# Kernel optimization log

Hardware: AMD Instinct MI355X
Metric: run time of the kernel (lower is better)

Reference implementation:

```python
import jax, jax.numpy as jnp
import numpy as np

B, T, V, D = 128, 512, 8000, 256
H = D // 2   # per-direction LSTM hidden
L = 4        # label_dim


def setup_inputs() -> dict:
    key = jax.random.key(0)
    ks = jax.random.split(key, 16)
    s = 0.1
    pad_seq = jax.random.randint(ks[0], (B, T), 0, V)
    lens = jax.random.randint(ks[1], (B,), 1, T + 1)
    lens = lens.at[0].set(T)  # padded length == max(lens), as pad_packed_sequence would give
    emb = (jax.random.normal(ks[2], (V, D)) * s).at[0].set(0.0)  # padding_idx=0
    return {
        "pad_seq": pad_seq, "lens": lens, "emb": emb,
        "W_ih_f": jax.random.normal(ks[3], (4 * H, D)) * s,
        "W_hh_f": jax.random.normal(ks[4], (4 * H, H)) * s,
        "b_ih_f": jax.random.normal(ks[5], (4 * H,)) * s,
        "b_hh_f": jax.random.normal(ks[6], (4 * H,)) * s,
        "W_ih_b": jax.random.normal(ks[7], (4 * H, D)) * s,
        "W_hh_b": jax.random.normal(ks[8], (4 * H, H)) * s,
        "b_ih_b": jax.random.normal(ks[9], (4 * H,)) * s,
        "b_hh_b": jax.random.normal(ks[10], (4 * H,)) * s,
        "W_lab": jax.random.normal(ks[11], (L, D)) * s,
        "b_lab": jax.random.normal(ks[12], (L,)) * s,
        "transitions": jax.random.normal(ks[13], (L, L)),
        "from_BOS": jax.random.normal(ks[14], (L,)),
        "to_EOS": jax.random.normal(ks[15], (L,)),
    }


def _lstm(xs_t, mask_t, Wih, Whh, bih, bhh, reverse):
    """Masked unidirectional LSTM over time-major xs_t [T,B,D]; emulates
    pack_padded_sequence semantics (state frozen and output zeroed at pads)."""
    nb, nh = xs_t.shape[1], Whh.shape[1]

    def step(carry, inp):
        h, c = carry
        x_t, m_t = inp  # [B,D], [B,1] bool
        g = x_t @ Wih.T + bih + h @ Whh.T + bhh
        i, f, gg, o = jnp.split(g, 4, axis=-1)
        c2 = jax.nn.sigmoid(f) * c + jax.nn.sigmoid(i) * jnp.tanh(gg)
        h2 = jax.nn.sigmoid(o) * jnp.tanh(c2)
        h = jnp.where(m_t, h2, h)
        c = jnp.where(m_t, c2, c)
        return (h, c), jnp.where(m_t, h2, 0.0)

    init = (jnp.zeros((nb, nh), xs_t.dtype), jnp.zeros((nb, nh), xs_t.dtype))
    _, ys = jax.lax.scan(step, init, (xs_t, mask_t), reverse=reverse)
    return ys  # [T,B,H]


def reference(pad_seq, lens, emb, W_ih_f, W_hh_f, b_ih_f, b_hh_f,
              W_ih_b, W_hh_b, b_ih_b, b_hh_b, W_lab, b_lab,
              transitions, from_BOS, to_EOS):
    b, t = pad_seq.shape
    x = emb[pad_seq]                       # [B,T,D]
    xs_t = jnp.transpose(x, (1, 0, 2))     # [T,B,D]
    mask_t = (jnp.arange(t)[:, None] < lens[None, :])[:, :, None]  # [T,B,1]

    hf = _lstm(xs_t, mask_t, W_ih_f, W_hh_f, b_ih_f, b_hh_f, reverse=False)
    hb = _lstm(xs_t, mask_t, W_ih_b, W_hh_b, b_ih_b, b_hh_b, reverse=True)
    h = jnp.concatenate([hf, hb], axis=-1)           # [T,B,D]
    scores = h @ W_lab.T + b_lab                     # [T,B,L] emissions

    # --- Viterbi forward pass ---
    best0 = from_BOS[None, :] + scores[0]            # [B,L]

    def vstep(best, inp):
        ti, e = inp                                  # step index, emissions [B,L]
        smat = best[:, :, None] + e[:, None, :] + transitions[None]  # [B,prev,cur]
        valid = (lens > ti)[:, None]
        nb = jnp.where(valid, smat.max(axis=1), best)
        return nb, jnp.argmax(smat, axis=1)          # backtrace [B,L]

    bestT, bt = jax.lax.scan(vstep, best0, (jnp.arange(1, t), scores[1:]))
    final_vec = bestT + to_EOS[None, :]              # [B,L]
    last_lab = jnp.argmax(final_vec, axis=1)         # [B]

    # --- backtrace: label[t] = bt[t][label[t+1]] for t < len-1 ---
    bt_pad = jnp.concatenate([bt, jnp.zeros((1,) + bt.shape[1:], bt.dtype)], axis=0)  # [T,B,L]

    def bstep(cur, inp):
        ti, bt_t = inp
        cand = jnp.take_along_axis(bt_t, cur[:, None], axis=1)[:, 0]
        cur = jnp.where(ti == lens - 1, last_lab,
                        jnp.where(ti < lens - 1, cand, cur))
        return cur, cur

    _, labs = jax.lax.scan(bstep, jnp.zeros((b,), last_lab.dtype),
                           (jnp.arange(t), bt_pad), reverse=True)
    labels = labs.T  # [B,T]
    len_bool = jnp.arange(t)[None, :] < lens[:, None]
    return labels * len_bool
```

## Files before the change

### kernel.cpp

```cpp
#include <hip/hip_runtime.h>
#include <math.h>

#define VOCAB 8000
#define BATCH 128
#define TMAX  512
#define DIM   256
#define HID   128
#define G4    512
#define NCOL  1024

__global__ __launch_bounds__(256) void embw_gemm(
    const float* __restrict__ emb,
    const float* __restrict__ Wf, const float* __restrict__ Wb,
    const float* __restrict__ bihf, const float* __restrict__ bhhf,
    const float* __restrict__ bihb, const float* __restrict__ bhhb,
    float* __restrict__ embW) {
  __shared__ float As[32][132];
  __shared__ float Bs[32][132];
  const int tid = threadIdx.x;
  const int m0 = blockIdx.x * 128;
  const int n0 = blockIdx.y * 128;
  const int tx = tid & 15, ty = tid >> 4;
  const int lrow = tid >> 1;
  const int lseg = (tid & 1) * 16;
  const float* Wsrc = (n0 < 512) ? Wf : Wb;
  const int nbase = (n0 < 512) ? n0 : (n0 - 512);

  float acc[8][8];
  #pragma unroll
  for (int i = 0; i < 8; ++i)
    #pragma unroll
    for (int jj = 0; jj < 8; ++jj) acc[i][jj] = 0.f;

  for (int k0 = 0; k0 < 256; k0 += 32) {
    const int gm = m0 + lrow;
    #pragma unroll
    for (int q = 0; q < 4; ++q) {
      float4 v = make_float4(0.f, 0.f, 0.f, 0.f);
      if (gm < VOCAB) v = *(const float4*)(emb + (size_t)gm * 256 + k0 + lseg + 4 * q);
      As[lseg + 4*q + 0][lrow] = v.x;
      As[lseg + 4*q + 1][lrow] = v.y;
      As[lseg + 4*q + 2][lrow] = v.z;
      As[lseg + 4*q + 3][lrow] = v.w;
    }
    #pragma unroll
    for (int q = 0; q < 4; ++q) {
      float4 v = *(const float4*)(Wsrc + (size_t)(nbase + lrow) * 256 + k0 + lseg + 4 * q);
      Bs[lseg + 4*q + 0][lrow] = v.x;
      Bs[lseg + 4*q + 1][lrow] = v.y;
      Bs[lseg + 4*q + 2][lrow] = v.z;
      Bs[lseg + 4*q + 3][lrow] = v.w;
    }
    __syncthreads();
    #pragma unroll
    for (int k = 0; k < 32; ++k) {
      float4 av0 = *(const float4*)&As[k][ty * 8];
      float4 av1 = *(const float4*)&As[k][ty * 8 + 4];
      float4 bv0 = *(const float4*)&Bs[k][tx * 4];
      float4 bv1 = *(const float4*)&Bs[k][64 + tx * 4];
      float a[8]  = {av0.x, av0.y, av0.z, av0.w, av1.x, av1.y, av1.z, av1.w};
      float bb[8] = {bv0.x, bv0.y, bv0.z, bv0.w, bv1.x, bv1.y, bv1.z, bv1.w};
      #pragma unroll
      for (int i = 0; i < 8; ++i)
        #pragma unroll
        for (int jj = 0; jj < 8; ++jj)
          acc[i][jj] += a[i] * bb[jj];
    }
    __syncthreads();
  }

  float bias[8];
  #pragma unroll
  for (int jj = 0; jj < 8; ++jj) {
    int n = n0 + ((jj < 4) ? (tx * 4 + jj) : (64 + tx * 4 + (jj - 4)));
    bias[jj] = (n < 512) ? (bihf[n] + bhhf[n]) : (bihb[n - 512] + bhhb[n - 512]);
  }
  #pragma unroll
  for (int i = 0; i < 8; ++i) {
    int gm = m0 + ty * 8 + i;
    if (gm >= VOCAB) continue;
    float4 v0 = make_float4(acc[i][0] + bias[0], acc[i][1] + bias[1],
                            acc[i][2] + bias[2], acc[i][3] + bias[3]);
    float4 v1 = make_float4(acc[i][4] + bias[4], acc[i][5] + bias[5],
                            acc[i][6] + bias[6], acc[i][7] + bias[7]);
    *(float4*)(embW + (size_t)gm * NCOL + n0 + tx * 4) = v0;
    *(float4*)(embW + (size_t)gm * NCOL + n0 + 64 + tx * 4) = v1;
  }
}

#define REP8(M) M(0) M(1) M(2) M(3) M(4) M(5) M(6) M(7)
#define REP8G(M,G) M(G,0) M(G,1) M(G,2) M(G,3) M(G,4) M(G,5) M(G,6) M(G,7)

__global__ __launch_bounds__(512)
__attribute__((amdgpu_waves_per_eu(2, 2)))
void lstm_rec(
    const int* __restrict__ pad_seq, const int* __restrict__ lens,
    const float* __restrict__ Whh_f, const float* __restrict__ Whh_b,
    const float* __restrict__ embW, const float* __restrict__ W_lab,
    float* __restrict__ e_part) {
  const int dir = blockIdx.x & 1;
  const int b   = blockIdx.x >> 1;
  const int tid = threadIdx.x;
  const int j   = tid >> 2;
  const int q   = tid & 3;
  const int parity = q & 1;
  const int half   = (q >> 1) & 1;

  __shared__ float ring[8][4][36];
  __shared__ float wls[4][132];
  __shared__ int   tok[TMAX];

  tok[tid] = pad_seq[b * TMAX + tid];
  wls[tid >> 7][tid & 127] = W_lab[(tid >> 7) * DIM + dir * HID + (tid & 127)];
  if (tid < 144) ((float*)ring)[tid] = 0.f;

  const int len = lens[b];
  const float* __restrict__ Whh = dir ? Whh_b : Whh_f;

  const float4* wr0 = (const float4*)(Whh + (size_t)(0 * HID + j) * HID + 32 * q);
  const float4* wr1 = (const float4*)(Whh + (size_t)(1 * HID + j) * HID + 32 * q);
  const float4* wr2 = (const float4*)(Whh + (size_t)(2 * HID + j) * HID + 32 * q);
  const float4* wr3 = (const float4*)(Whh + (size_t)(3 * HID + j) * HID + 32 * q);
#define DECLW(G,I)                                                      \
  float w##G##_##I##_0, w##G##_##I##_1, w##G##_##I##_2, w##G##_##I##_3; \
  { float4 t = wr##G[I];                                                \
    w##G##_##I##_0 = t.x; w##G##_##I##_1 = t.y;                         \
    w##G##_##I##_2 = t.z; w##G##_##I##_3 = t.w; }                       \
  asm volatile("" : "+v"(w##G##_##I##_0));                              \
  asm volatile("" : "+v"(w##G##_##I##_1));                              \
  asm volatile("" : "+v"(w##G##_##I##_2));                              \
  asm volatile("" : "+v"(w##G##_##I##_3));
  REP8G(DECLW,0) REP8G(DECLW,1) REP8G(DECLW,2) REP8G(DECLW,3)
#undef DECLW

  float c = 0.f;
  const float ascale = (q == 2) ? 2.f : 1.f;
  const float* __restrict__ ecol = embW + dir * G4 + (q * HID + j);
  float* __restrict__ ep = e_part + (size_t)(dir * BATCH + b) * TMAX * 4;

  __syncthreads();

  float xb0, xb1, xb2, xb3, xb4, xb5, xb6, xb7;
#define PRE(r) { const int ss = nbase + r; xb##r = 0.f;                 \
    if (ss < len) {                                                     \
      const int tt = dir ? (len - 1 - ss) : ss;                         \
      xb##r = ecol[(size_t)tok[tt] * NCOL]; } }
  { const int nbase = 0; REP8(PRE) }

#define MACC(G,I)                                         \
    a##G##0 = fmaf(hv##I.x, w##G##_##I##_0, a##G##0);     \
    a##G##1 = fmaf(hv##I.y, w##G##_##I##_1, a##G##1);     \
    a##G##2 = fmaf(hv##I.z, w##G##_##I##_2, a##G##2);     \
    a##G##3 = fmaf(hv##I.w, w##G##_##I##_3, a##G##3);

#define STEP(r, XW)                                                     \
  {                                                                     \
    const float4* h4 = (const float4*)&ring[r][q][0];                   \
    float4 hv0 = h4[0], hv1 = h4[1], hv2 = h4[2], hv3 = h4[3];          \
    float4 hv4 = h4[4], hv5 = h4[5], hv6 = h4[6], hv7 = h4[7];          \
    float a00=0.f,a01=0.f,a02=0.f,a03=0.f;                              \
    float a10=0.f,a11=0.f,a12=0.f,a13=0.f;                              \
    float a20=0.f,a21=0.f,a22=0.f,a23=0.f;                              \
    float a30=0.f,a31=0.f,a32=0.f,a33=0.f;                              \
    REP8G(MACC,0) REP8G(MACC,1) REP8G(MACC,2) REP8G(MACC,3)             \
    const float p0 = (a00+a01)+(a02+a03);                               \
    const float p1 = (a10+a11)+(a12+a13);                               \
    const float p2 = (a20+a21)+(a22+a23);                               \
    const float p3 = (a30+a31)+(a32+a33);                               \
          \
    const float klo = parity ? p1 : p0, slo = parity ? p0 : p1;         \
    const float khi = parity ? p3 : p2, shi = parity ? p2 : p3;         \
    const float alo = klo + __shfl_xor(slo, 1);                         \
    const float ahi = khi + __shfl_xor(shi, 1);                         \
    const float kb = half ? ahi : alo, sb = half ? alo : ahi;           \
    const float tot = kb + __shfl_xor(sb, 2);                           \
    const float aa = tot + (XW);                                        \
    const float sg = 1.f / (1.f + __expf(-ascale * aa));                \
    const float act = (q == 2) ? (2.f * sg - 1.f) : sg;                 \
    const float e1 = __shfl_xor(act, 1);                                \
    const float e2 = __shfl_xor(act, 2);                                \
    const float e3 = __shfl_xor(e1, 2);                                 \
    const float ev  = parity ? e1 : act, od  = parity ? act : e1;       \
    const float ev2 = parity ? e3 : e2,  od2 = parity ? e2 : e3;        \
    const float ig = half ? ev2 : ev, fg = half ? od2 : od;             \
    const float gt = half ? ev : ev2, og = half ? od : od2;             \
    c = fg * c + ig * gt;                                               \
    const float s2 = 1.f / (1.f + __expf(-2.f * c));                    \
    const float hh = og * (2.f * s2 - 1.f);                             \
    if (q == 0) ring[(r + 1) & 7][j >> 5][j & 31] = hh;                 \
    __syncthreads();                                                    \
  }

  for (int s0 = 0; s0 < len; s0 += 8) {
    const int cnt = (len - s0 < 8) ? (len - s0) : 8;
    STEP(0, xb0)
    if (cnt > 1) STEP(1, xb1)
    if (cnt > 2) STEP(2, xb2)
    if (cnt > 3) STEP(3, xb3)
    if (cnt > 4) STEP(4, xb4)
    if (cnt > 5) STEP(5, xb5)
    if (cnt > 6) STEP(6, xb6)
    if (cnt > 7) STEP(7, xb7)
    { const int nbase = s0 + 8; REP8(PRE) }
    {
      const int r = tid >> 6, l = (tid >> 4) & 3, sub = tid & 15;
      if (r < cnt) {
        const float4* hp = (const float4*)&ring[(r + 1) & 7][sub >> 2][8 * (sub & 3)];
        const float4 h0 = hp[0], h1 = hp[1];
        const float4* wp = (const float4*)&wls[l][8 * sub];
        const float4 u0 = wp[0], u1 = wp[1];
        float d = h0.x*u0.x + h0.y*u0.y + h0.z*u0.z + h0.w*u0.w
                + h1.x*u1.x + h1.y*u1.y + h1.z*u1.z + h1.w*u1.w;
        d += __shfl_xor(d, 1); d += __shfl_xor(d, 2);
        d += __shfl_xor(d, 4); d += __shfl_xor(d, 8);
        if (sub == 0) {
          const int ss = s0 + r;
          const int tt = dir ? (len - 1 - ss) : ss;
          ep[tt * 4 + l] = d;
        }
      }
    }
    asm volatile("" : "+v"(xb0), "+v"(xb1), "+v"(xb2), "+v"(xb3),
                      "+v"(xb4), "+v"(xb5), "+v"(xb6), "+v"(xb7));
    __syncthreads();
  }
#undef STEP
#undef MACC
#undef PRE
}

__global__ __launch_bounds__(512) void viterbi_k(
    const int* __restrict__ lens, const float* __restrict__ e_part,
    const float* __restrict__ b_lab, const float* __restrict__ trans,
    const float* __restrict__ from_BOS, const float* __restrict__ to_EOS,
    int* __restrict__ out) {
  const int b = blockIdx.x;
  const int tid = threadIdx.x;
  __shared__ float sc[TMAX][4];
  __shared__ unsigned btm[TMAX];
  __shared__ int labs[TMAX];
  const int len = lens[b];

  if (tid < len) {
    const float4 f  = *(const float4*)(e_part + ((size_t)b * TMAX + tid) * 4);
    const float4 g2 = *(const float4*)(e_part + ((size_t)(BATCH + b) * TMAX + tid) * 4);
    const float4 bl = *(const float4*)b_lab;
    sc[tid][0] = f.x + g2.x + bl.x;
    sc[tid][1] = f.y + g2.y + bl.y;
    sc[tid][2] = f.z + g2.z + bl.z;
    sc[tid][3] = f.w + g2.w + bl.w;
  }
  __syncthreads();

  if (tid < 4) {
    const int l = tid;
    float trc0 = trans[0 * 4 + l], trc1 = trans[1 * 4 + l];
    float trc2 = trans[2 * 4 + l], trc3 = trans[3 * 4 + l];
    float best = from_BOS[l] + sc[0][l];
    float e_next = sc[1][l];
    for (int ti = 1; ti < len; ++ti) {
      const float e = e_next;
      e_next = sc[(ti + 1 < TMAX) ? ti + 1 : ti][l];
      const float b0 = __shfl(best, 0);
      const float b1 = __shfl(best, 1);
      const float b2 = __shfl(best, 2);
      const float b3 = __shfl(best, 3);
      float m = (b0 + e) + trc0; int arg = 0;
      float v;
      v = (b1 + e) + trc1; if (v > m) { m = v; arg = 1; }
      v = (b2 + e) + trc2; if (v > m) { m = v; arg = 2; }
      v = (b3 + e) + trc3; if (v > m) { m = v; arg = 3; }
      best = m;
      unsigned av = ((unsigned)arg) << (8 * l);
      av |= __shfl_xor(av, 1);
      av |= __shfl_xor(av, 2);
      if (l == 0) btm[ti] = av;
    }
    const float f0 = __shfl(best, 0) + to_EOS[0];
    const float f1 = __shfl(best, 1) + to_EOS[1];
    const float f2 = __shfl(best, 2) + to_EOS[2];
    const float f3 = __shfl(best, 3) + to_EOS[3];
    if (l == 0) {
      float m = f0; int last = 0;
      if (f1 > m) { m = f1; last = 1; }
      if (f2 > m) { m = f2; last = 2; }
      if (f3 > m) { m = f3; last = 3; }
      labs[len - 1] = last;
      int cur = last;
      #pragma unroll 4
      for (int ti = len - 2; ti >= 0; --ti) {
        cur = (int)((btm[ti + 1] >> (8 * cur)) & 255u);
        labs[ti] = cur;
      }
    }
  }
  __syncthreads();
  out[b * TMAX + tid] = (tid < len) ? labs[tid] : 0;
}

extern "C" void kernel_launch(void* const* d_in, const int* in_sizes, int n_in,
                              void* d_out, int out_size, void* d_ws, size_t ws_size,
                              hipStream_t stream) {
  const int*   pad_seq  = (const int*)d_in[0];
  const int*   lens     = (const int*)d_in[1];
  const float* emb      = (const float*)d_in[2];
  const float* W_ih_f   = (const float*)d_in[3];
  const float* W_hh_f   = (const float*)d_in[4];
  const float* b_ih_f   = (const float*)d_in[5];
  const float* b_hh_f   = (const float*)d_in[6];
  const float* W_ih_b   = (const float*)d_in[7];
  const float* W_hh_b   = (const float*)d_in[8];
  const float* b_ih_b   = (const float*)d_in[9];
  const float* b_hh_b   = (const float*)d_in[10];
  const float* W_lab    = (const float*)d_in[11];
  const float* b_lab    = (const float*)d_in[12];
  const float* trans    = (const float*)d_in[13];
  const float* from_BOS = (const float*)d_in[14];
  const float* to_EOS   = (const float*)d_in[15];
  int* out = (int*)d_out;

  float* embW   = (float*)d_ws;
  float* e_part = embW + (size_t)VOCAB * NCOL;

  embw_gemm<<<dim3(63, 8), 256, 0, stream>>>(emb, W_ih_f, W_ih_b,
                                             b_ih_f, b_hh_f, b_ih_b, b_hh_b, embW);
  lstm_rec<<<dim3(2 * BATCH), 512, 0, stream>>>(pad_seq, lens, W_hh_f, W_hh_b,
                                                embW, W_lab, e_part);
  viterbi_k<<<dim3(BATCH), 512, 0, stream>>>(lens, e_part, b_lab, trans,
                                             from_BOS, to_EOS, out);
}
```

Baseline: 628.9 us.

## Use packed FP32 FMA in the GEMM and LSTM recurrence, simplify gate reduction

Switches the embedding-weight GEMM inner product and the LSTM hidden-state matvec to two-wide float vectors so the compiler can emit packed FP32 FMAs (v_pk_fma_f32), halving the FMA instruction count. The recurrent weights are pinned in register pairs through double bitcasts. The gate reduction no longer uses parity/half select shuffles. Every lane now butterfly-reduces all four gate sums with 8 shuffles and computes all four activations redundantly, instead of one activation followed by a redistribution. This trades more shuffles and transcendentals per lane for fewer selects and a shorter dependency chain on the serial recurrence path.

```diff
diff --git a/kernel.cpp b/kernel.cpp
--- a/kernel.cpp
+++ b/kernel.cpp
@@ -8,6 +8,16 @@
 #define HID   128
 #define G4    512
 #define NCOL  1024
+
+typedef float v2f __attribute__((ext_vector_type(2)));
+
+__device__ __forceinline__ v2f fma2(v2f a, v2f b, v2f c) {
+#if __has_builtin(__builtin_elementwise_fma)
+  return __builtin_elementwise_fma(a, b, c);
+#else
+  v2f r; r.x = fmaf(a.x, b.x, c.x); r.y = fmaf(a.y, b.y, c.y); return r;
+#endif
+}
 
 __global__ __launch_bounds__(256) void embw_gemm(
     const float* __restrict__ emb,
@@ -26,11 +36,11 @@
   const float* Wsrc = (n0 < 512) ? Wf : Wb;
   const int nbase = (n0 < 512) ? n0 : (n0 - 512);
 
-  float acc[8][8];
+  v2f acc2[8][4];
   #pragma unroll
   for (int i = 0; i < 8; ++i)
     #pragma unroll
-    for (int jj = 0; jj < 8; ++jj) acc[i][jj] = 0.f;
+    for (int jj = 0; jj < 4; ++jj) { acc2[i][jj].x = 0.f; acc2[i][jj].y = 0.f; }
 
   for (int k0 = 0; k0 < 256; k0 += 32) {
     const int gm = m0 + lrow;
@@ -58,13 +68,18 @@
       float4 av1 = *(const float4*)&As[k][ty * 8 + 4];
       float4 bv0 = *(const float4*)&Bs[k][tx * 4];
       float4 bv1 = *(const float4*)&Bs[k][64 + tx * 4];
-      float a[8]  = {av0.x, av0.y, av0.z, av0.w, av1.x, av1.y, av1.z, av1.w};
-      float bb[8] = {bv0.x, bv0.y, bv0.z, bv0.w, bv1.x, bv1.y, bv1.z, bv1.w};
+      float a8[8] = {av0.x, av0.y, av0.z, av0.w, av1.x, av1.y, av1.z, av1.w};
+      v2f b20, b21, b22, b23;
+      b20.x = bv0.x; b20.y = bv0.y;  b21.x = bv0.z; b21.y = bv0.w;
+      b22.x = bv1.x; b22.y = bv1.y;  b23.x = bv1.z; b23.y = bv1.w;
       #pragma unroll
-      for (int i = 0; i < 8; ++i)
-        #pragma unroll
-        for (int jj = 0; jj < 8; ++jj)
-          acc[i][jj] += a[i] * bb[jj];
+      for (int i = 0; i < 8; ++i) {
+        v2f ai; ai.x = a8[i]; ai.y = a8[i];
+        acc2[i][0] = fma2(ai, b20, acc2[i][0]);
+        acc2[i][1] = fma2(ai, b21, acc2[i][1]);
+        acc2[i][2] = fma2(ai, b22, acc2[i][2]);
+        acc2[i][3] = fma2(ai, b23, acc2[i][3]);
+      }
     }
     __syncthreads();
   }
@@ -79,17 +94,21 @@
   for (int i = 0; i < 8; ++i) {
     int gm = m0 + ty * 8 + i;
     if (gm >= VOCAB) continue;
-    float4 v0 = make_float4(acc[i][0] + bias[0], acc[i][1] + bias[1],
-                            acc[i][2] + bias[2], acc[i][3] + bias[3]);
-    float4 v1 = make_float4(acc[i][4] + bias[4], acc[i][5] + bias[5],
-                            acc[i][6] + bias[6], acc[i][7] + bias[7]);
+    float4 v0 = make_float4(acc2[i][0].x + bias[0], acc2[i][0].y + bias[1],
+                            acc2[i][1].x + bias[2], acc2[i][1].y + bias[3]);
+    float4 v1 = make_float4(acc2[i][2].x + bias[4], acc2[i][2].y + bias[5],
+                            acc2[i][3].x + bias[6], acc2[i][3].y + bias[7]);
     *(float4*)(embW + (size_t)gm * NCOL + n0 + tx * 4) = v0;
     *(float4*)(embW + (size_t)gm * NCOL + n0 + 64 + tx * 4) = v1;
   }
 }
 
 #define REP8(M) M(0) M(1) M(2) M(3) M(4) M(5) M(6) M(7)
-#define REP8G(M,G) M(G,0) M(G,1) M(G,2) M(G,3) M(G,4) M(G,5) M(G,6) M(G,7)
+#define REPD(M,G) M(G,0,0,1) M(G,1,2,3) M(G,2,4,5) M(G,3,6,7) \
+                  M(G,4,8,9) M(G,5,10,11) M(G,6,12,13) M(G,7,14,15)
+#define REPM(M,G) M(G,0,A) M(G,1,B) M(G,2,A) M(G,3,B) M(G,4,A) M(G,5,B) \
+  M(G,6,A) M(G,7,B) M(G,8,A) M(G,9,B) M(G,10,A) M(G,11,B) M(G,12,A) \
+  M(G,13,B) M(G,14,A) M(G,15,B)
 
 __global__ __launch_bounds__(512)
 __attribute__((amdgpu_waves_per_eu(2, 2)))
@@ -103,8 +122,6 @@
   const int tid = threadIdx.x;
   const int j   = tid >> 2;
   const int q   = tid & 3;
-  const int parity = q & 1;
-  const int half   = (q >> 1) & 1;
 
   __shared__ float ring[8][4][36];
   __shared__ float wls[4][132];
@@ -121,20 +138,21 @@
   const float4* wr1 = (const float4*)(Whh + (size_t)(1 * HID + j) * HID + 32 * q);
   const float4* wr2 = (const float4*)(Whh + (size_t)(2 * HID + j) * HID + 32 * q);
   const float4* wr3 = (const float4*)(Whh + (size_t)(3 * HID + j) * HID + 32 * q);
-#define DECLW(G,I)                                                      \
-  float w##G##_##I##_0, w##G##_##I##_1, w##G##_##I##_2, w##G##_##I##_3; \
+#define DECLW(G,I,PA,PB)                                                \
+  v2f wp##G##_##PA, wp##G##_##PB;                                       \
   { float4 t = wr##G[I];                                                \
-    w##G##_##I##_0 = t.x; w##G##_##I##_1 = t.y;                         \
-    w##G##_##I##_2 = t.z; w##G##_##I##_3 = t.w; }                       \
-  asm volatile("" : "+v"(w##G##_##I##_0));                              \
-  asm volatile("" : "+v"(w##G##_##I##_1));                              \
-  asm volatile("" : "+v"(w##G##_##I##_2));                              \
-  asm volatile("" : "+v"(w##G##_##I##_3));
-  REP8G(DECLW,0) REP8G(DECLW,1) REP8G(DECLW,2) REP8G(DECLW,3)
+    v2f vA; vA.x = t.x; vA.y = t.y;                                     \
+    v2f vB; vB.x = t.z; vB.y = t.w;                                     \
+    double dA = __builtin_bit_cast(double, vA);                         \
+    double dB = __builtin_bit_cast(double, vB);                         \
+    asm volatile("" : "+v"(dA));                                        \
+    asm volatile("" : "+v"(dB));                                        \
+    wp##G##_##PA = __builtin_bit_cast(v2f, dA);                         \
+    wp##G##_##PB = __builtin_bit_cast(v2f, dB); }
+  REPD(DECLW,0) REPD(DECLW,1) REPD(DECLW,2) REPD(DECLW,3)
 #undef DECLW
 
   float c = 0.f;
-  const float ascale = (q == 2) ? 2.f : 1.f;
   const float* __restrict__ ecol = embW + dir * G4 + (q * HID + j);
   float* __restrict__ ep = e_part + (size_t)(dir * BATCH + b) * TMAX * 4;
 
@@ -147,43 +165,42 @@
       xb##r = ecol[(size_t)tok[tt] * NCOL]; } }
   { const int nbase = 0; REP8(PRE) }
 
-#define MACC(G,I)                                         \
-    a##G##0 = fmaf(hv##I.x, w##G##_##I##_0, a##G##0);     \
-    a##G##1 = fmaf(hv##I.y, w##G##_##I##_1, a##G##1);     \
-    a##G##2 = fmaf(hv##I.z, w##G##_##I##_2, a##G##2);     \
-    a##G##3 = fmaf(hv##I.w, w##G##_##I##_3, a##G##3);
+#define MACC(G,K,AB) ac##G##AB = fma2(hp##K, wp##G##_##K, ac##G##AB);
+#define HPAIR(K,F,S0,S1) v2f hp##K; hp##K.x = F.S0; hp##K.y = F.S1;
 
 #define STEP(r, XW)                                                     \
   {                                                                     \
     const float4* h4 = (const float4*)&ring[r][q][0];                   \
-    float4 hv0 = h4[0], hv1 = h4[1], hv2 = h4[2], hv3 = h4[3];          \
-    float4 hv4 = h4[4], hv5 = h4[5], hv6 = h4[6], hv7 = h4[7];          \
-    float a00=0.f,a01=0.f,a02=0.f,a03=0.f;                              \
-    float a10=0.f,a11=0.f,a12=0.f,a13=0.f;                              \
-    float a20=0.f,a21=0.f,a22=0.f,a23=0.f;                              \
-    float a30=0.f,a31=0.f,a32=0.f,a33=0.f;                              \
-    REP8G(MACC,0) REP8G(MACC,1) REP8G(MACC,2) REP8G(MACC,3)             \
-    const float p0 = (a00+a01)+(a02+a03);                               \
-    const float p1 = (a10+a11)+(a12+a13);                               \
-    const float p2 = (a20+a21)+(a22+a23);                               \
-    const float p3 = (a30+a31)+(a32+a33);                               \
-          \
-    const float klo = parity ? p1 : p0, slo = parity ? p0 : p1;         \
-    const float khi = parity ? p3 : p2, shi = parity ? p2 : p3;         \
-    const float alo = klo + __shfl_xor(slo, 1);                         \
-    const float ahi = khi + __shfl_xor(shi, 1);                         \
-    const float kb = half ? ahi : alo, sb = half ? alo : ahi;           \
-    const float tot = kb + __shfl_xor(sb, 2);                           \
-    const float aa = tot + (XW);                                        \
-    const float sg = 1.f / (1.f + __expf(-ascale * aa));                \
-    const float act = (q == 2) ? (2.f * sg - 1.f) : sg;                 \
-    const float e1 = __shfl_xor(act, 1);                                \
-    const float e2 = __shfl_xor(act, 2);                                \
-    const float e3 = __shfl_xor(e1, 2);                                 \
-    const float ev  = parity ? e1 : act, od  = parity ? act : e1;       \
-    const float ev2 = parity ? e3 : e2,  od2 = parity ? e2 : e3;        \
-    const float ig = half ? ev2 : ev, fg = half ? od2 : od;             \
-    const float gt = half ? ev : ev2, og = half ? od : od2;             \
+    float4 f0=h4[0], f1=h4[1], f2=h4[2], f3=h4[3];                      \
+    float4 f4=h4[4], f5=h4[5], f6=h4[6], f7=h4[7];                      \
+    HPAIR(0,f0,x,y)  HPAIR(1,f0,z,w)  HPAIR(2,f1,x,y)  HPAIR(3,f1,z,w)  \
+    HPAIR(4,f2,x,y)  HPAIR(5,f2,z,w)  HPAIR(6,f3,x,y)  HPAIR(7,f3,z,w)  \
+    HPAIR(8,f4,x,y)  HPAIR(9,f4,z,w)  HPAIR(10,f5,x,y) HPAIR(11,f5,z,w) \
+    HPAIR(12,f6,x,y) HPAIR(13,f6,z,w) HPAIR(14,f7,x,y) HPAIR(15,f7,z,w) \
+    v2f ac0A = {0.f,0.f}, ac0B = {0.f,0.f};                             \
+    v2f ac1A = {0.f,0.f}, ac1B = {0.f,0.f};                             \
+    v2f ac2A = {0.f,0.f}, ac2B = {0.f,0.f};                             \
+    v2f ac3A = {0.f,0.f}, ac3B = {0.f,0.f};                             \
+    REPM(MACC,0) REPM(MACC,1) REPM(MACC,2) REPM(MACC,3)                 \
+    float p0 = (ac0A.x + ac0A.y) + (ac0B.x + ac0B.y);                   \
+    float p1 = (ac1A.x + ac1A.y) + (ac1B.x + ac1B.y);                   \
+    float p2 = (ac2A.x + ac2A.y) + (ac2B.x + ac2B.y);                   \
+    float p3 = (ac3A.x + ac3A.y) + (ac3B.x + ac3B.y);                   \
+     \
+    p0 += (q == 0) ? (XW) : 0.f;                                        \
+    p1 += (q == 1) ? (XW) : 0.f;                                        \
+    p2 += (q == 2) ? (XW) : 0.f;                                        \
+    p3 += (q == 3) ? (XW) : 0.f;                                        \
+                     \
+    p0 += __shfl_xor(p0, 1); p1 += __shfl_xor(p1, 1);                   \
+    p2 += __shfl_xor(p2, 1); p3 += __shfl_xor(p3, 1);                   \
+    p0 += __shfl_xor(p0, 2); p1 += __shfl_xor(p1, 2);                   \
+    p2 += __shfl_xor(p2, 2); p3 += __shfl_xor(p3, 2);                   \
+    const float ig = 1.f / (1.f + __expf(-p0));                         \
+    const float fg = 1.f / (1.f + __expf(-p1));                         \
+    const float sgg = 1.f / (1.f + __expf(-2.f * p2));                  \
+    const float gt = 2.f * sgg - 1.f;                                   \
+    const float og = 1.f / (1.f + __expf(-p3));                         \
     c = fg * c + ig * gt;                                               \
     const float s2 = 1.f / (1.f + __expf(-2.f * c));                    \
     const float hh = og * (2.f * s2 - 1.f);                             \
@@ -226,6 +243,7 @@
   }
 #undef STEP
 #undef MACC
+#undef HPAIR
 #undef PRE
 }
 
```

After: 725.2 us. +15.3%, slower.
